# Kernel tuning notes

Measured on AMD Instinct MI355X. Metric: run time of the kernel, lower is better.

Reference implementation:

```python
import jax, jax.numpy as jnp
import numpy as np

TEMPERATURE = 0.1
NUM_CLASSES = 21
L2_EPS = 1e-12   # torch F.normalize eps
NEG = -1e9       # masking value for invalid (absent-class) logit slots


def setup_inputs() -> dict:
    key = jax.random.key(0)
    k1, k2 = jax.random.split(key)
    features = jax.random.normal(k1, (16, 512, 64, 64), dtype=jnp.float32)
    labels = jax.random.randint(k2, (16, 513, 513), 0, NUM_CLASSES, dtype=jnp.int32)
    return {"features": features, "labels": labels}


def reference(features, labels):
    B, D, H, W = features.shape
    C = NUM_CLASSES
    # torch: F.interpolate(labels.float()[:,None], (H,W), mode='bilinear').squeeze(1).long()
    lab = jax.image.resize(labels.astype(jnp.float32)[:, None], (B, 1, H, W),
                           method="bilinear", antialias=False)
    lab = lab[:, 0].astype(jnp.int32)                     # [B,H,W]

    # per-image, per-class masked feature pooling (segment reduce)
    masks = (lab[:, None, :, :] == jnp.arange(C)[None, :, None, None]).astype(features.dtype)  # [B,C,H,W]
    sums = jnp.einsum('bdhw,bchw->bcd', features, masks)  # [B,C,D]
    norms = jnp.linalg.norm(sums, axis=-1, keepdims=True)
    protos = sums / jnp.maximum(norms, L2_EPS)            # normalized prototypes [B,C,D]
    pres = masks.sum((2, 3)) > 0                          # [B,C] class present in image

    # all pairwise prototype dots: S[c,e,i,j] = <proto[i,c], proto[j,e]> / T
    S = jnp.einsum('icd,jed->ceij', protos, protos) / TEMPERATURE  # [C,C,B,B]
    presT = pres.T                                        # [C,B]
    valid = presT[:, None, :, None] & presT[None, :, None, :]       # [C,C,B,B]
    masked = jnp.where(valid, S, NEG)

    idx = jnp.arange(C)
    diag = masked[idx, idx]                               # [C,B,B] positive block S[c,c]
    dvalid = valid[idx, idx]                              # [C,B,B]

    # logits for class c = concat(p_block, all n_blocks) -> diag block appears twice
    lse_diag = jax.nn.logsumexp(diag, axis=(1, 2))        # [C]
    lse_all = jax.nn.logsumexp(masked, axis=(1, 2, 3))    # [C]
    lse = jnp.logaddexp(lse_diag, lse_all)                # [C]

    cnt = dvalid.sum((1, 2))
    pos_mean = jnp.where(dvalid, diag, 0.0).sum((1, 2)) / jnp.maximum(cnt, 1)

    cls_present = pres.any(0)                             # [C]
    loss = jnp.sum(jnp.where(cls_present, lse - pos_mean, 0.0))
    return loss
```

## Files before the change

kernel.cpp:

```cpp
#include <hip/hip_runtime.h>
#include <cstdint>
#include <cstddef>

#define NUM_C 21
#define NROW 336

__global__ __launch_bounds__(256) void k1_resize_hist(const int* __restrict__ labels,
                                                      uint8_t* __restrict__ lab,
                                                      int* __restrict__ counts,
                                                      float* __restrict__ out) {
    int b = blockIdx.x;
    if (b == 0 && threadIdx.x == 0) out[0] = 0.0f;
    __shared__ int hist[NUM_C];
    if (threadIdx.x < NUM_C) hist[threadIdx.x] = 0;
    __syncthreads();
    const int* L = labels + (size_t)b * 513 * 513;
    uint8_t* labB = lab + b * 4096;
    for (int it = 0; it < 16; ++it) {
        int p = it * 256 + threadIdx.x;
        int y = p >> 6, x = p & 63;
        float sy = (y + 0.5f) * 8.015625f - 0.5f;
        float sx = (x + 0.5f) * 8.015625f - 0.5f;
        int y0 = (int)sy; float fy = sy - (float)y0;
        int x0 = (int)sx; float fx = sx - (float)x0;
        const int* r0 = L + y0 * 513 + x0;
        float L00 = (float)r0[0],   L01 = (float)r0[1];
        float L10 = (float)r0[513], L11 = (float)r0[514];
        float v0 = (1.0f - fx) * L00 + fx * L01;
        float v1 = (1.0f - fx) * L10 + fx * L11;
        float val = (1.0f - fy) * v0 + fy * v1;
        int c = (int)val;
        labB[p] = (uint8_t)c;
        atomicAdd(&hist[c], 1);
    }
    __syncthreads();
    if (threadIdx.x < NUM_C) counts[b * NUM_C + threadIdx.x] = hist[threadIdx.x];
}

__global__ __launch_bounds__(256) void k2_sums(const float* __restrict__ feat,
                                               const uint8_t* __restrict__ lab,
                                               float* __restrict__ sums) {
    int b  = blockIdx.x >> 7;
    int dg = blockIdx.x & 127;
    int t = threadIdx.x;
    int wv = t >> 6, lane = t & 63;
    __shared__ uint8_t labLds[4096];
    __shared__ float accum[4][NUM_C * 64];

    const uint32_t* labSrc = (const uint32_t*)(lab + b * 4096);
    uint32_t* labDst = (uint32_t*)labLds;
#pragma unroll
    for (int q = 0; q < 4; ++q) labDst[t + 256 * q] = labSrc[t + 256 * q];

    float* accFlat = &accum[0][0];
#pragma unroll
    for (int q = 0; q < NUM_C; ++q) accFlat[t + 256 * q] = 0.0f;
    __syncthreads();

    int d = dg * 4 + wv;
    const float* f = feat + ((size_t)(b * 512 + d)) * 4096;
    float* acc = accum[wv];
#pragma unroll 4
    for (int it = 0; it < 64; ++it) {
        int p = it * 64 + lane;
        float v = f[p];
        int c = labLds[p];
        acc[c * 64 + lane] += v;
    }
    for (int c = 0; c < NUM_C; ++c) {
        float v = acc[c * 64 + lane];
#pragma unroll
        for (int off = 32; off >= 1; off >>= 1) v += __shfl_xor(v, off, 64);
        if (lane == 0) sums[(size_t)(c * 16 + b) * 512 + d] = v;
    }
}

__global__ __launch_bounds__(256) void k3_norms(const float* __restrict__ sums,
                                                float* __restrict__ invn) {
    int w = blockIdx.x * 4 + (threadIdx.x >> 6);
    int lane = threadIdx.x & 63;
    if (w >= NROW) return;
    const float4* s4 = (const float4*)(sums + (size_t)w * 512);
    float ss = 0.0f;
#pragma unroll
    for (int q = 0; q < 2; ++q) {
        float4 v = s4[lane + 64 * q];
        ss += v.x * v.x + v.y * v.y + v.z * v.z + v.w * v.w;
    }
#pragma unroll
    for (int off = 32; off >= 1; off >>= 1) ss += __shfl_xor(ss, off, 64);
    if (lane == 0) invn[w] = 1.0f / fmaxf(sqrtf(ss), 1e-12f);
}

__global__ __launch_bounds__(64) void k4_gram(const float* __restrict__ sums,
                                              float* __restrict__ gpart) {
    int row0 = blockIdx.x * 32, col0 = blockIdx.y * 32, k0 = blockIdx.z * 64;
    __shared__ float A[32 * 66], Bt[32 * 66];
    int t = threadIdx.x;
    int row = t >> 1, kk0 = (t & 1) * 32;
#pragma unroll
    for (int q = 0; q < 8; ++q) {
        int kk = kk0 + q * 4;
        int ra = row0 + row, rb = col0 + row;
        float4 va = (ra < NROW) ? *(const float4*)&sums[(size_t)ra * 512 + k0 + kk]
                                : make_float4(0.f, 0.f, 0.f, 0.f);
        float4 vb = (rb < NROW) ? *(const float4*)&sums[(size_t)rb * 512 + k0 + kk]
                                : make_float4(0.f, 0.f, 0.f, 0.f);
        *(float2*)&A[row * 66 + kk]      = make_float2(va.x, va.y);
        *(float2*)&A[row * 66 + kk + 2]  = make_float2(va.z, va.w);
        *(float2*)&Bt[row * 66 + kk]     = make_float2(vb.x, vb.y);
        *(float2*)&Bt[row * 66 + kk + 2] = make_float2(vb.z, vb.w);
    }
    __syncthreads();
    int ty = t >> 3, tx = t & 7;
    float acc[4][4] = {};
    for (int kk = 0; kk < 64; kk += 2) {
        float2 a[4], bb[4];
#pragma unroll
        for (int u = 0; u < 4; ++u) {
            a[u]  = *(const float2*)&A[(ty * 4 + u) * 66 + kk];
            bb[u] = *(const float2*)&Bt[(tx * 4 + u) * 66 + kk];
        }
#pragma unroll
        for (int u = 0; u < 4; ++u)
#pragma unroll
            for (int v = 0; v < 4; ++v)
                acc[u][v] += a[u].x * bb[v].x + a[u].y * bb[v].y;
    }
    float* gp = gpart + (size_t)blockIdx.z * (NROW * NROW);
#pragma unroll
    for (int u = 0; u < 4; ++u) {
        int r1 = row0 + ty * 4 + u;
        if (r1 >= NROW) continue;
#pragma unroll
        for (int v = 0; v < 4; ++v) {
            int r2 = col0 + tx * 4 + v;
            if (r2 < NROW) gp[(size_t)r1 * NROW + r2] = acc[u][v];
        }
    }
}

__global__ __launch_bounds__(256) void k5_loss(const float* __restrict__ gpart,
                                               const float* __restrict__ invn,
                                               const int* __restrict__ counts,
                                               float* __restrict__ out) {
    int c = blockIdx.x;
    int t = threadIdx.x;
    int wv = t >> 6, lane = t & 63;
    __shared__ float sRows[16 * NROW];
    __shared__ float invnL[NROW];
    __shared__ uint8_t presL[NROW];
    __shared__ float redM[4], redE[4], redD[4], redL[4];

    for (int r = t; r < NROW; r += 256) {
        invnL[r] = invn[r];
        int img = r & 15, cls = r >> 4;
        presL[r] = (counts[img * NUM_C + cls] > 0) ? 1 : 0;
    }
    __syncthreads();

    for (int i = 0; i < 16; ++i) {
        int r1 = c * 16 + i;
        bool rowValid = presL[r1] != 0;
        float in1 = invnL[r1];
        for (int r2 = t; r2 < NROW; r2 += 256) {
            float acc = 0.0f;
#pragma unroll
            for (int s = 0; s < 8; ++s)
                acc += gpart[(size_t)s * (NROW * NROW) + (size_t)r1 * NROW + r2];
            float sval = acc * in1 * invnL[r2] * 10.0f;
            sRows[i * NROW + r2] = (rowValid && presL[r2]) ? sval : -1e30f;
        }
    }
    __syncthreads();

    float m = -1e30f;
    for (int idx = t; idx < 16 * NROW; idx += 256) m = fmaxf(m, sRows[idx]);
#pragma unroll
    for (int off = 32; off >= 1; off >>= 1) m = fmaxf(m, __shfl_xor(m, off, 64));
    if (lane == 0) redM[wv] = m;
    __syncthreads();
    m = fmaxf(fmaxf(redM[0], redM[1]), fmaxf(redM[2], redM[3]));

    int nc = 0;
    for (int j = 0; j < 16; ++j) nc += presL[c * 16 + j];
    if (nc == 0) return;

    float expSum = 0.0f, diagExp = 0.0f, diagLin = 0.0f;
    int dlo = c * 16, dhi = c * 16 + 16;
    for (int i = 0; i < 16; ++i) {
        for (int r2 = t; r2 < NROW; r2 += 256) {
            float s = sRows[i * NROW + r2];
            float e = expf(s - m);
            expSum += e;
            if (r2 >= dlo && r2 < dhi && s > -1e29f) { diagExp += e; diagLin += s; }
        }
    }
#pragma unroll
    for (int off = 32; off >= 1; off >>= 1) {
        expSum  += __shfl_xor(expSum, off, 64);
        diagExp += __shfl_xor(diagExp, off, 64);
        diagLin += __shfl_xor(diagLin, off, 64);
    }
    if (lane == 0) { redE[wv] = expSum; redD[wv] = diagExp; redL[wv] = diagLin; }
    __syncthreads();
    if (t == 0) {
        float E = redE[0] + redE[1] + redE[2] + redE[3];
        float D = redD[0] + redD[1] + redD[2] + redD[3];
        float Ln = redL[0] + redL[1] + redL[2] + redL[3];
        float lse = m + logf(E + D);
        float posMean = Ln / (float)(nc * nc);
        atomicAdd(out, lse - posMean);
    }
}

extern "C" void kernel_launch(void* const* d_in, const int* in_sizes, int n_in,
                              void* d_out, int out_size, void* d_ws, size_t ws_size,
                              hipStream_t stream) {
    const float* features = (const float*)d_in[0];
    const int* labels = (const int*)d_in[1];
    char* ws = (char*)d_ws;

    uint8_t* lab  = (uint8_t*)ws;
    int* counts   = (int*)(ws + 65536);
    float* sums   = (float*)(ws + 65536 + 2048);
    float* invn   = (float*)(ws + 65536 + 2048 + 688128);
    float* gpart  = (float*)(ws + 65536 + 2048 + 688128 + 2048);
    float* out    = (float*)d_out;

    k1_resize_hist<<<16, 256, 0, stream>>>(labels, lab, counts, out);
    k2_sums<<<2048, 256, 0, stream>>>(features, lab, sums);
    k3_norms<<<84, 256, 0, stream>>>(sums, invn);
    k4_gram<<<dim3(11, 11, 8), 64, 0, stream>>>(sums, gpart);
    k5_loss<<<21, 256, 0, stream>>>(gpart, invn, counts, out);
}
```

Baseline: 254.8 us.

## Split resize across more blocks, vectorize sums, fold norms into loss

```diff
diff --git a/kernel.cpp b/kernel.cpp
--- a/kernel.cpp
+++ b/kernel.cpp
@@ -4,37 +4,36 @@
 
 #define NUM_C 21
 #define NROW 336
+#define N2   (NROW * NROW)
 
 __global__ __launch_bounds__(256) void k1_resize_hist(const int* __restrict__ labels,
                                                       uint8_t* __restrict__ lab,
-                                                      int* __restrict__ counts,
+                                                      int* __restrict__ countsPart,
                                                       float* __restrict__ out) {
-    int b = blockIdx.x;
-    if (b == 0 && threadIdx.x == 0) out[0] = 0.0f;
+    int b = blockIdx.x >> 4, strip = blockIdx.x & 15;
+    if (blockIdx.x == 0 && threadIdx.x == 0) out[0] = 0.0f;
     __shared__ int hist[NUM_C];
     if (threadIdx.x < NUM_C) hist[threadIdx.x] = 0;
     __syncthreads();
-    const int* L = labels + (size_t)b * 513 * 513;
-    uint8_t* labB = lab + b * 4096;
-    for (int it = 0; it < 16; ++it) {
-        int p = it * 256 + threadIdx.x;
-        int y = p >> 6, x = p & 63;
-        float sy = (y + 0.5f) * 8.015625f - 0.5f;
-        float sx = (x + 0.5f) * 8.015625f - 0.5f;
-        int y0 = (int)sy; float fy = sy - (float)y0;
-        int x0 = (int)sx; float fx = sx - (float)x0;
-        const int* r0 = L + y0 * 513 + x0;
-        float L00 = (float)r0[0],   L01 = (float)r0[1];
-        float L10 = (float)r0[513], L11 = (float)r0[514];
-        float v0 = (1.0f - fx) * L00 + fx * L01;
-        float v1 = (1.0f - fx) * L10 + fx * L11;
-        float val = (1.0f - fy) * v0 + fy * v1;
-        int c = (int)val;
-        labB[p] = (uint8_t)c;
-        atomicAdd(&hist[c], 1);
-    }
-    __syncthreads();
-    if (threadIdx.x < NUM_C) counts[b * NUM_C + threadIdx.x] = hist[threadIdx.x];
+
+    int p = strip * 256 + threadIdx.x;
+    int y = p >> 6, x = p & 63;
+    const int* L = labels + (size_t)b * 263169;
+    float sy = (y + 0.5f) * 8.015625f - 0.5f;
+    float sx = (x + 0.5f) * 8.015625f - 0.5f;
+    int y0 = (int)sy; float fy = sy - (float)y0;
+    int x0 = (int)sx; float fx = sx - (float)x0;
+    const int* r0 = L + y0 * 513 + x0;
+    float L00 = (float)r0[0],   L01 = (float)r0[1];
+    float L10 = (float)r0[513], L11 = (float)r0[514];
+    float v0 = (1.0f - fx) * L00 + fx * L01;
+    float v1 = (1.0f - fx) * L10 + fx * L11;
+    float val = (1.0f - fy) * v0 + fy * v1;
+    int c = (int)val;
+    lab[b * 4096 + p] = (uint8_t)c;
+    atomicAdd(&hist[c], 1);
+    __syncthreads();
+    if (threadIdx.x < NUM_C) countsPart[blockIdx.x * NUM_C + threadIdx.x] = hist[threadIdx.x];
 }
 
 __global__ __launch_bounds__(256) void k2_sums(const float* __restrict__ feat,
@@ -44,28 +43,29 @@
     int dg = blockIdx.x & 127;
     int t = threadIdx.x;
     int wv = t >> 6, lane = t & 63;
-    __shared__ uint8_t labLds[4096];
+    __shared__ uint32_t lab4[1024];
     __shared__ float accum[4][NUM_C * 64];
 
     const uint32_t* labSrc = (const uint32_t*)(lab + b * 4096);
-    uint32_t* labDst = (uint32_t*)labLds;
-#pragma unroll
-    for (int q = 0; q < 4; ++q) labDst[t + 256 * q] = labSrc[t + 256 * q];
-
+#pragma unroll
+    for (int q = 0; q < 4; ++q) lab4[t + 256 * q] = labSrc[t + 256 * q];
     float* accFlat = &accum[0][0];
 #pragma unroll
     for (int q = 0; q < NUM_C; ++q) accFlat[t + 256 * q] = 0.0f;
     __syncthreads();
 
     int d = dg * 4 + wv;
-    const float* f = feat + ((size_t)(b * 512 + d)) * 4096;
+    const float4* f4 = (const float4*)(feat + ((size_t)(b * 512 + d)) * 4096);
     float* acc = accum[wv];
 #pragma unroll 4
-    for (int it = 0; it < 64; ++it) {
-        int p = it * 64 + lane;
-        float v = f[p];
-        int c = labLds[p];
-        acc[c * 64 + lane] += v;
+    for (int it = 0; it < 16; ++it) {
+        int p4 = it * 64 + lane;
+        float4 v = f4[p4];
+        uint32_t l4 = lab4[p4];
+        acc[(l4 & 255u) * 64 + lane]         += v.x;
+        acc[((l4 >> 8) & 255u) * 64 + lane]  += v.y;
+        acc[((l4 >> 16) & 255u) * 64 + lane] += v.z;
+        acc[(l4 >> 24) * 64 + lane]          += v.w;
     }
     for (int c = 0; c < NUM_C; ++c) {
         float v = acc[c * 64 + lane];
@@ -73,23 +73,6 @@
         for (int off = 32; off >= 1; off >>= 1) v += __shfl_xor(v, off, 64);
         if (lane == 0) sums[(size_t)(c * 16 + b) * 512 + d] = v;
     }
-}
-
-__global__ __launch_bounds__(256) void k3_norms(const float* __restrict__ sums,
-                                                float* __restrict__ invn) {
-    int w = blockIdx.x * 4 + (threadIdx.x >> 6);
-    int lane = threadIdx.x & 63;
-    if (w >= NROW) return;
-    const float4* s4 = (const float4*)(sums + (size_t)w * 512);
-    float ss = 0.0f;
-#pragma unroll
-    for (int q = 0; q < 2; ++q) {
-        float4 v = s4[lane + 64 * q];
-        ss += v.x * v.x + v.y * v.y + v.z * v.z + v.w * v.w;
-    }
-#pragma unroll
-    for (int off = 32; off >= 1; off >>= 1) ss += __shfl_xor(ss, off, 64);
-    if (lane == 0) invn[w] = 1.0f / fmaxf(sqrtf(ss), 1e-12f);
 }
 
 __global__ __launch_bounds__(64) void k4_gram(const float* __restrict__ sums,
@@ -127,7 +110,7 @@
             for (int v = 0; v < 4; ++v)
                 acc[u][v] += a[u].x * bb[v].x + a[u].y * bb[v].y;
     }
-    float* gp = gpart + (size_t)blockIdx.z * (NROW * NROW);
+    float* gp = gpart + (size_t)blockIdx.z * N2;
 #pragma unroll
     for (int u = 0; u < 4; ++u) {
         int r1 = row0 + ty * 4 + u;
@@ -140,75 +123,60 @@
     }
 }
 
-__global__ __launch_bounds__(256) void k5_loss(const float* __restrict__ gpart,
-                                               const float* __restrict__ invn,
-                                               const int* __restrict__ counts,
+__global__ __launch_bounds__(512) void k5_loss(const float* __restrict__ gpart,
+                                               const int* __restrict__ countsPart,
                                                float* __restrict__ out) {
-    int c = blockIdx.x;
-    int t = threadIdx.x;
+    int c = blockIdx.x, t = threadIdx.x;
     int wv = t >> 6, lane = t & 63;
-    __shared__ float sRows[16 * NROW];
     __shared__ float invnL[NROW];
     __shared__ uint8_t presL[NROW];
-    __shared__ float redM[4], redE[4], redD[4], redL[4];
-
-    for (int r = t; r < NROW; r += 256) {
-        invnL[r] = invn[r];
+    __shared__ float redE[8], redD[8], redL[8];
+
+    for (int r = t; r < NROW; r += 512) {
+        float ss = 0.0f;
+#pragma unroll
+        for (int s = 0; s < 8; ++s) ss += gpart[(size_t)s * N2 + (size_t)r * 337];
+        invnL[r] = 1.0f / fmaxf(sqrtf(ss), 1e-12f);
         int img = r & 15, cls = r >> 4;
-        presL[r] = (counts[img * NUM_C + cls] > 0) ? 1 : 0;
-    }
-    __syncthreads();
-
-    for (int i = 0; i < 16; ++i) {
-        int r1 = c * 16 + i;
-        bool rowValid = presL[r1] != 0;
-        float in1 = invnL[r1];
-        for (int r2 = t; r2 < NROW; r2 += 256) {
-            float acc = 0.0f;
-#pragma unroll
-            for (int s = 0; s < 8; ++s)
-                acc += gpart[(size_t)s * (NROW * NROW) + (size_t)r1 * NROW + r2];
-            float sval = acc * in1 * invnL[r2] * 10.0f;
-            sRows[i * NROW + r2] = (rowValid && presL[r2]) ? sval : -1e30f;
-        }
-    }
-    __syncthreads();
-
-    float m = -1e30f;
-    for (int idx = t; idx < 16 * NROW; idx += 256) m = fmaxf(m, sRows[idx]);
-#pragma unroll
-    for (int off = 32; off >= 1; off >>= 1) m = fmaxf(m, __shfl_xor(m, off, 64));
-    if (lane == 0) redM[wv] = m;
-    __syncthreads();
-    m = fmaxf(fmaxf(redM[0], redM[1]), fmaxf(redM[2], redM[3]));
+        int cnt = 0;
+#pragma unroll
+        for (int s = 0; s < 16; ++s) cnt += countsPart[(img * 16 + s) * NUM_C + cls];
+        presL[r] = cnt > 0 ? 1 : 0;
+    }
+    __syncthreads();
 
     int nc = 0;
+#pragma unroll
     for (int j = 0; j < 16; ++j) nc += presL[c * 16 + j];
     if (nc == 0) return;
 
-    float expSum = 0.0f, diagExp = 0.0f, diagLin = 0.0f;
-    int dlo = c * 16, dhi = c * 16 + 16;
-    for (int i = 0; i < 16; ++i) {
-        for (int r2 = t; r2 < NROW; r2 += 256) {
-            float s = sRows[i * NROW + r2];
-            float e = expf(s - m);
-            expSum += e;
-            if (r2 >= dlo && r2 < dhi && s > -1e29f) { diagExp += e; diagLin += s; }
+    float eS = 0.0f, dE = 0.0f, dL = 0.0f;
+    for (int idx = t; idx < 16 * NROW; idx += 512) {
+        int i = idx / NROW, r2 = idx - i * NROW;
+        int r1 = c * 16 + i;
+        float g = 0.0f;
+#pragma unroll
+        for (int s = 0; s < 8; ++s) g += gpart[(size_t)s * N2 + (size_t)r1 * NROW + r2];
+        if (presL[r1] && presL[r2]) {
+            float sv = g * invnL[r1] * invnL[r2] * 10.0f;
+            float e = expf(sv - 10.0f);
+            eS += e;
+            if ((r2 >> 4) == c) { dE += e; dL += sv; }
         }
     }
 #pragma unroll
     for (int off = 32; off >= 1; off >>= 1) {
-        expSum  += __shfl_xor(expSum, off, 64);
-        diagExp += __shfl_xor(diagExp, off, 64);
-        diagLin += __shfl_xor(diagLin, off, 64);
-    }
-    if (lane == 0) { redE[wv] = expSum; redD[wv] = diagExp; redL[wv] = diagLin; }
+        eS += __shfl_xor(eS, off, 64);
+        dE += __shfl_xor(dE, off, 64);
+        dL += __shfl_xor(dL, off, 64);
+    }
+    if (lane == 0) { redE[wv] = eS; redD[wv] = dE; redL[wv] = dL; }
     __syncthreads();
     if (t == 0) {
-        float E = redE[0] + redE[1] + redE[2] + redE[3];
-        float D = redD[0] + redD[1] + redD[2] + redD[3];
-        float Ln = redL[0] + redL[1] + redL[2] + redL[3];
-        float lse = m + logf(E + D);
+        float E = 0, D = 0, Ln = 0;
+#pragma unroll
+        for (int w = 0; w < 8; ++w) { E += redE[w]; D += redD[w]; Ln += redL[w]; }
+        float lse = 10.0f + logf(E + D);
         float posMean = Ln / (float)(nc * nc);
         atomicAdd(out, lse - posMean);
     }
@@ -221,16 +189,14 @@
     const int* labels = (const int*)d_in[1];
     char* ws = (char*)d_ws;
 
-    uint8_t* lab  = (uint8_t*)ws;
-    int* counts   = (int*)(ws + 65536);
-    float* sums   = (float*)(ws + 65536 + 2048);
-    float* invn   = (float*)(ws + 65536 + 2048 + 688128);
-    float* gpart  = (float*)(ws + 65536 + 2048 + 688128 + 2048);
-    float* out    = (float*)d_out;
-
-    k1_resize_hist<<<16, 256, 0, stream>>>(labels, lab, counts, out);
+    uint8_t* lab    = (uint8_t*)ws;
+    int* countsPart = (int*)(ws + 65536);
+    float* sums     = (float*)(ws + 65536 + 21504);
+    float* gpart    = (float*)(ws + 65536 + 21504 + 688128);
+    float* out      = (float*)d_out;
+
+    k1_resize_hist<<<256, 256, 0, stream>>>(labels, lab, countsPart, out);
     k2_sums<<<2048, 256, 0, stream>>>(features, lab, sums);
-    k3_norms<<<84, 256, 0, stream>>>(sums, invn);
     k4_gram<<<dim3(11, 11, 8), 64, 0, stream>>>(sums, gpart);
-    k5_loss<<<21, 256, 0, stream>>>(gpart, invn, counts, out);
-}
+    k5_loss<<<21, 512, 0, stream>>>(gpart, countsPart, out);
+}
```

Measured after the change: 231.3 us. 9.2% less time.
